# Performance work log

Hardware: AMD Instinct MI355X
Metric: run time of the kernel (lower is better)

## Reference

```python
import jax, jax.numpy as jnp
import numpy as np

B, N, C = 4, 2048, 512
H = 8  # num_heads
HD = C // H  # head_dim = 64


def setup_inputs() -> dict:
    key = jax.random.key(0)
    k_x, k_qkv, k_w, k_b = jax.random.split(key, 4)
    x = jax.random.normal(k_x, (B, N, C), dtype=jnp.float32)
    # torch nn.Linear weights are stored as (out_features, in_features)
    w_qkv = jax.random.normal(k_qkv, (3 * C, C), dtype=jnp.float32) * 0.02  # bias=False
    w_proj = jax.random.normal(k_w, (C, C), dtype=jnp.float32) * 0.02
    b_proj = jax.random.normal(k_b, (C,), dtype=jnp.float32) * 0.02
    return {"x": x, "w_qkv": w_qkv, "w_proj": w_proj, "b_proj": b_proj}


def reference(x, w_qkv, w_proj, b_proj):
    b, n, c = x.shape
    scale = HD ** -0.5
    # QKV projection (no bias): (B,N,C) @ (C,3C) -> (B,N,3C)
    qkv = jnp.einsum('bnc,dc->bnd', x, w_qkv)
    qkv = qkv.reshape(b, n, 3, H, HD).transpose(2, 0, 3, 1, 4)  # (3,B,H,N,HD)
    q, k, v = qkv[0], qkv[1], qkv[2]
    # scaled dot-product attention, full N x N scores
    attn = jnp.einsum('bhqd,bhkd->bhqk', q, k) * scale
    attn = jax.nn.softmax(attn, axis=-1)
    out = jnp.einsum('bhqk,bhkd->bhqd', attn, v)  # (B,H,N,HD)
    out = out.transpose(0, 2, 1, 3).reshape(b, n, c)  # (B,N,C)
    # output projection with bias
    return jnp.einsum('bnc,dc->bnd', out, w_proj) + b_proj
```

## Files before the change

kernel.cpp:

```cpp
#include <hip/hip_runtime.h>

typedef _Float16 f16;
typedef _Float16 f16x4 __attribute__((ext_vector_type(4)));
typedef _Float16 f16x8 __attribute__((ext_vector_type(8)));
typedef __fp16 fp16x2 __attribute__((ext_vector_type(2)));
typedef float f32x4 __attribute__((ext_vector_type(4)));

static __device__ __forceinline__ f32x4 mfma_k32(f16x8 a, f16x8 b, f32x4 c) {
  return __builtin_amdgcn_mfma_f32_16x16x32_f16(a, b, c, 0, 0, 0);
}
static __device__ __forceinline__ f32x4 mfma_k16(f16x4 a, f16x4 b, f32x4 c) {
  return __builtin_amdgcn_mfma_f32_16x16x16f16(a, b, c, 0, 0, 0);
}
static __device__ __forceinline__ void gll16(const f16* g, f16* l) {
  __builtin_amdgcn_global_load_lds(
      (const __attribute__((address_space(1))) void*)g,
      (__attribute__((address_space(3))) void*)l, 16, 0, 0);
}

#define BN 2048
#define CC 512
#define NHD 64
#define MROWS 8192
#define SLAB ((size_t)32 * BN * NHD)
#define CH 64
#define QSCALE 0.1803368801111204f

__global__ __launch_bounds__(256)
void cvt_f16(const float* __restrict__ X, const float* __restrict__ Wq,
             const float* __restrict__ Wp, f16* __restrict__ x16,
             f16* __restrict__ wq16, f16* __restrict__ wp16) {
  const int idx = blockIdx.x * 256 + threadIdx.x;
  const int stride = gridDim.x * 256;
  for (int i = idx; i < (MROWS * CC) / 4; i += stride) {
    float4 v = ((const float4*)X)[i];
    f16x4 h = {(f16)v.x, (f16)v.y, (f16)v.z, (f16)v.w};
    ((f16x4*)x16)[i] = h;
  }
  for (int i = idx; i < (3 * CC * CC) / 4; i += stride) {
    float4 v = ((const float4*)Wq)[i];
    f16x4 h = {(f16)v.x, (f16)v.y, (f16)v.z, (f16)v.w};
    ((f16x4*)wq16)[i] = h;
  }
  for (int i = idx; i < (CC * CC) / 4; i += stride) {
    float4 v = ((const float4*)Wp)[i];
    f16x4 h = {(f16)v.x, (f16)v.y, (f16)v.z, (f16)v.w};
    ((f16x4*)wp16)[i] = h;
  }
}

__global__ __launch_bounds__(256)
void qkv_gemm(const f16* __restrict__ X, const f16* __restrict__ W,
              f16* __restrict__ qkv) {
  __shared__ __align__(16) f16 As[128 * 32];
  __shared__ __align__(16) f16 Bs[128 * 32];
  const int t = threadIdx.x;
  const int lane = t & 63, wave = t >> 6;
  const int wr = wave >> 1, wc = wave & 1;
  const int mt = blockIdx.x / 12, nt = blockIdx.x % 12;
  const int m0 = mt * 128, n0 = nt * 128;
  const int grp = lane >> 4, lid = lane & 15;

  const int srow = 32 * wave + (lane >> 2);
  const int gslot = (lane & 3) ^ ((lane >> 2) & 3);
  const int ga0 = (m0 + srow) * CC + gslot * 8;
  const int gb0 = (n0 + srow) * CC + gslot * 8;
  f16* const ldsA = As + wave * 1024;
  f16* const ldsB = Bs + wave * 1024;

  const int abase = wr * 2048 + lid * 32 + (grp ^ (lid & 3)) * 8;
  const int bbase = wc * 2048 + lid * 32 + (grp ^ (lid & 3)) * 8;

  const f32x4 zf = {0.f, 0.f, 0.f, 0.f};
  f32x4 acc[4][4];
#pragma unroll
  for (int i = 0; i < 4; i++)
#pragma unroll
    for (int j = 0; j < 4; j++) acc[i][j] = zf;

  for (int k0 = 0; k0 < CC; k0 += 32) {
    gll16(X + ga0 + k0, ldsA);
    gll16(X + ga0 + 16 * CC + k0, ldsA + 512);
    gll16(W + gb0 + k0, ldsB);
    gll16(W + gb0 + 16 * CC + k0, ldsB + 512);
    __syncthreads();
    f16x8 af[4], bf[4];
#pragma unroll
    for (int mi = 0; mi < 4; mi++)
      af[mi] = *(const f16x8*)&As[abase + mi * 512];
#pragma unroll
    for (int ni = 0; ni < 4; ni++)
      bf[ni] = *(const f16x8*)&Bs[bbase + ni * 512];
#pragma unroll
    for (int mi = 0; mi < 4; mi++)
#pragma unroll
      for (int ni = 0; ni < 4; ni++)
        acc[mi][ni] = mfma_k32(af[mi], bf[ni], acc[mi][ni]);
    __syncthreads();
  }
#pragma unroll
  for (int ni = 0; ni < 4; ni++) {
    int d = n0 + wc * 64 + ni * 16 + lid;
    int s = d >> 9;
    int h = (d & 511) >> 6;
    int hd = d & 63;
    if (s == 2) {
#pragma unroll
      for (int mi = 0; mi < 4; mi++) {
        int row0 = m0 + wr * 64 + mi * 16 + grp * 4;
        int b = row0 >> 11, n = row0 & 2047;
        f16x4 pk = {(f16)acc[mi][ni][0], (f16)acc[mi][ni][1],
                    (f16)acc[mi][ni][2], (f16)acc[mi][ni][3]};
        *(f16x4*)&qkv[2 * SLAB + ((size_t)((b * 8 + h) * 64 + hd)) * BN + n] = pk;
      }
    } else {
      float scale = (s == 0) ? QSCALE : 1.0f;
#pragma unroll
      for (int mi = 0; mi < 4; mi++) {
#pragma unroll
        for (int i = 0; i < 4; i++) {
          int row = m0 + wr * 64 + mi * 16 + grp * 4 + i;
          int b = row >> 11, n = row & 2047;
          qkv[(size_t)s * SLAB + (((size_t)(b * 8 + h) * BN + n)) * NHD + hd] =
              (f16)(acc[mi][ni][i] * scale);
        }
      }
    }
  }
}

__global__ __launch_bounds__(256)
void attn(const f16* __restrict__ qkv, f16* __restrict__ O) {
  __shared__ __align__(16) char smem[32768];

  const int bh = blockIdx.x & 31;
  const int qb = blockIdx.x >> 5;
  const f16* Q = qkv + (size_t)bh * BN * NHD;
  const f16* K = qkv + SLAB + (size_t)bh * BN * NHD;
  const f16* VT = qkv + 2 * SLAB + (size_t)bh * (size_t)NHD * BN;
  const int t = threadIdx.x, lane = t & 63, wave = t >> 6;
  const int grp = lane >> 4, qv = lane & 15;
  const int qrow0 = qb * 128 + wave * 32 + qv;
  const int xr = (qv & 7) << 4;

  char* const kaddr0 = smem + qv * 128 + ((grp * 16) ^ xr);
  char* const kaddr1 = smem + qv * 128 + ((grp * 16 + 64) ^ xr);
  char* const va0 = smem + qv * 128 + ((0 * 32 + grp * 8) ^ xr);
  char* const va1 = smem + qv * 128 + ((1 * 32 + grp * 8) ^ xr);
  char* const va2 = smem + qv * 128 + ((2 * 32 + grp * 8) ^ xr);
  char* const va3 = smem + qv * 128 + ((3 * 32 + grp * 8) ^ xr);

  const int r0 = t >> 3, cb = t & 7, r1 = r0 + 32;
  const int lo_k0 = r0 * NHD + cb * 8;
  const int lo_k1 = r1 * NHD + cb * 8;
  const int lo_v0 = r0 * BN + cb * 8;
  const int lo_v1 = r1 * BN + cb * 8;
  char* const waddr0 = smem + ((r0 * 128 + cb * 16) ^ ((r0 & 7) << 4));
  char* const waddr1 = smem + ((r1 * 128 + cb * 16) ^ ((r1 & 7) << 4));

  f16x8 qfA0 = *(const f16x8*)(Q + (size_t)qrow0 * NHD + grp * 8);
  f16x8 qfA1 = *(const f16x8*)(Q + (size_t)qrow0 * NHD + 32 + grp * 8);
  f16x8 qfB0 = *(const f16x8*)(Q + (size_t)(qrow0 + 16) * NHD + grp * 8);
  f16x8 qfB1 = *(const f16x8*)(Q + (size_t)(qrow0 + 16) * NHD + 32 + grp * 8);

  const f32x4 zf = {0.f, 0.f, 0.f, 0.f};
  const f16x4 ones = {(f16)1.f, (f16)1.f, (f16)1.f, (f16)1.f};
  f32x4 accA[4], accB[4];
#pragma unroll
  for (int i = 0; i < 4; i++) { accA[i] = zf; accB[i] = zf; }
  f32x4 laccA = zf, laccB = zf;

  int koff = 0, voff = 0;
  {
    f16x8 sk0 = *(const f16x8*)(K + lo_k0);
    f16x8 sk1 = *(const f16x8*)(K + lo_k1);
    f16x8 sv0 = *(const f16x8*)(VT + lo_v0);
    f16x8 sv1 = *(const f16x8*)(VT + lo_v1);
    koff = CH * NHD; voff = CH;
    *(f16x8*)(waddr0) = sk0;
    *(f16x8*)(waddr1) = sk1;
    *(f16x8*)(waddr0 + 16384) = sv0;
    *(f16x8*)(waddr1 + 16384) = sv1;
  }
  __syncthreads();

#define ATTN_BODY(BUF, PF)                                                    \
  {                                                                           \
    f16x8 sk0, sk1, sv0, sv1;                                                 \
    if (PF) {                                                                 \
      sk0 = *(const f16x8*)(K + koff + lo_k0);                                \
      sk1 = *(const f16x8*)(K + koff + lo_k1);                                \
      sv0 = *(const f16x8*)(VT + voff + lo_v0);                               \
      sv1 = *(const f16x8*)(VT + voff + lo_v1);                               \
      koff += CH * NHD; voff += CH;                                           \
    }                                                                         \
    __builtin_amdgcn_s_setprio(1);                                            \
    _Pragma("unroll")                                                         \
    for (int kt = 0; kt < 4; kt++) {                                          \
      f16x8 k0v = *(const f16x8*)(kaddr0 + BUF * 8192 + kt * 2048);           \
      f16x8 k1v = *(const f16x8*)(kaddr1 + BUF * 8192 + kt * 2048);           \
      f32x4 stA = mfma_k32(k1v, qfA1, mfma_k32(k0v, qfA0, zf));               \
      f32x4 stB = mfma_k32(k1v, qfB1, mfma_k32(k0v, qfB0, zf));               \
      union { f16x4 v; fp16x2 h[2]; } uA, uB;                                 \
      uA.h[0] = __builtin_amdgcn_cvt_pkrtz(exp2f(stA[0]), exp2f(stA[1]));     \
      uA.h[1] = __builtin_amdgcn_cvt_pkrtz(exp2f(stA[2]), exp2f(stA[3]));     \
      uB.h[0] = __builtin_amdgcn_cvt_pkrtz(exp2f(stB[0]), exp2f(stB[1]));     \
      uB.h[1] = __builtin_amdgcn_cvt_pkrtz(exp2f(stB[2]), exp2f(stB[3]));     \
      f16x4 pbA = uA.v, pbB = uB.v;                                           \
      laccA = mfma_k16(ones, pbA, laccA);                                     \
      laccB = mfma_k16(ones, pbB, laccB);                                     \
      const char* vak = (kt == 0) ? va0 : (kt == 1) ? va1 : (kt == 2) ? va2 : va3; \
      _Pragma("unroll")                                                       \
      for (int dt = 0; dt < 4; dt++) {                                        \
        f16x4 vf = *(const f16x4*)(vak + 16384 + BUF * 8192 + dt * 2048);     \
        accA[dt] = mfma_k16(vf, pbA, accA[dt]);                               \
        accB[dt] = mfma_k16(vf, pbB, accB[dt]);                               \
      }                                                                       \
    }                                                                         \
    __builtin_amdgcn_s_setprio(0);                                            \
    if (PF) {                                                                 \
      *(f16x8*)(waddr0 + (BUF ^ 1) * 8192) = sk0;                             \
      *(f16x8*)(waddr1 + (BUF ^ 1) * 8192) = sk1;                             \
      *(f16x8*)(waddr0 + 16384 + (BUF ^ 1) * 8192) = sv0;                     \
      *(f16x8*)(waddr1 + 16384 + (BUF ^ 1) * 8192) = sv1;                     \
    }                                                                         \
    __syncthreads();                                                          \
  }

  for (int p = 0; p < 15; ++p) {
    ATTN_BODY(0, 1)
    ATTN_BODY(1, 1)
  }
  ATTN_BODY(0, 1)
  ATTN_BODY(1, 0)
#undef ATTN_BODY

  const int b = bh >> 3, h = bh & 7;
  {
    float inv = 1.0f / laccA[0];
#pragma unroll
    for (int dt = 0; dt < 4; dt++) {
      f16x4 o = {(f16)(accA[dt][0] * inv), (f16)(accA[dt][1] * inv),
                 (f16)(accA[dt][2] * inv), (f16)(accA[dt][3] * inv)};
      *(f16x4*)&O[((size_t)(b * BN + qrow0)) * CC + h * NHD + dt * 16 + grp * 4] = o;
    }
  }
  {
    float inv = 1.0f / laccB[0];
#pragma unroll
    for (int dt = 0; dt < 4; dt++) {
      f16x4 o = {(f16)(accB[dt][0] * inv), (f16)(accB[dt][1] * inv),
                 (f16)(accB[dt][2] * inv), (f16)(accB[dt][3] * inv)};
      *(f16x4*)&O[((size_t)(b * BN + qrow0 + 16)) * CC + h * NHD + dt * 16 + grp * 4] = o;
    }
  }
}

__global__ __launch_bounds__(256)
void proj_gemm(const f16* __restrict__ A, const f16* __restrict__ W,
               const float* __restrict__ bias, float* __restrict__ out) {
  __shared__ __align__(16) f16 As[128 * 32];
  __shared__ __align__(16) f16 Bs[128 * 32];
  const int t = threadIdx.x;
  const int lane = t & 63, wave = t >> 6;
  const int wr = wave >> 1, wc = wave & 1;
  const int mt = blockIdx.x >> 2, nt = blockIdx.x & 3;
  const int m0 = mt * 128, n0 = nt * 128;
  const int grp = lane >> 4, lid = lane & 15;

  const int srow = 32 * wave + (lane >> 2);
  const int gslot = (lane & 3) ^ ((lane >> 2) & 3);
  const int ga0 = (m0 + srow) * CC + gslot * 8;
  const int gb0 = (n0 + srow) * CC + gslot * 8;
  f16* const ldsA = As + wave * 1024;
  f16* const ldsB = Bs + wave * 1024;
  const int abase = wr * 2048 + lid * 32 + (grp ^ (lid & 3)) * 8;
  const int bbase = wc * 2048 + lid * 32 + (grp ^ (lid & 3)) * 8;

  const f32x4 zf = {0.f, 0.f, 0.f, 0.f};
  f32x4 acc[4][4];
#pragma unroll
  for (int i = 0; i < 4; i++)
#pragma unroll
    for (int j = 0; j < 4; j++) acc[i][j] = zf;

  for (int k0 = 0; k0 < CC; k0 += 32) {
    gll16(A + ga0 + k0, ldsA);
    gll16(A + ga0 + 16 * CC + k0, ldsA + 512);
    gll16(W + gb0 + k0, ldsB);
    gll16(W + gb0 + 16 * CC + k0, ldsB + 512);
    __syncthreads();
    f16x8 af[4], bf[4];
#pragma unroll
    for (int mi = 0; mi < 4; mi++)
      af[mi] = *(const f16x8*)&As[abase + mi * 512];
#pragma unroll
    for (int ni = 0; ni < 4; ni++)
      bf[ni] = *(const f16x8*)&Bs[bbase + ni * 512];
#pragma unroll
    for (int mi = 0; mi < 4; mi++)
#pragma unroll
      for (int ni = 0; ni < 4; ni++)
        acc[mi][ni] = mfma_k32(af[mi], bf[ni], acc[mi][ni]);
    __syncthreads();
  }
#pragma unroll
  for (int mi = 0; mi < 4; mi++) {
#pragma unroll
    for (int ni = 0; ni < 4; ni++) {
      int d = n0 + wc * 64 + ni * 16 + lid;
      float bv = bias[d];
#pragma unroll
      for (int i = 0; i < 4; i++) {
        int row = m0 + wr * 64 + mi * 16 + grp * 4 + i;
        out[(size_t)row * CC + d] = acc[mi][ni][i] + bv;
      }
    }
  }
}

extern "C" void kernel_launch(void* const* d_in, const int* in_sizes, int n_in,
                              void* d_out, int out_size, void* d_ws, size_t ws_size,
                              hipStream_t stream) {
  const float* x = (const float*)d_in[0];
  const float* w_qkv = (const float*)d_in[1];
  const float* w_proj = (const float*)d_in[2];
  const float* b_proj = (const float*)d_in[3];
  float* out = (float*)d_out;

  f16* qkv = (f16*)d_ws;
  f16* Obuf = qkv + 3 * SLAB;
  f16* x16 = Obuf;
  f16* wq16 = Obuf + (size_t)MROWS * CC;
  f16* wp16 = wq16 + (size_t)3 * CC * CC;

  cvt_f16<<<dim3(1024), dim3(256), 0, stream>>>(x, w_qkv, w_proj, x16, wq16, wp16);
  qkv_gemm<<<dim3(64 * 12), dim3(256), 0, stream>>>(x16, wq16, qkv);
  attn<<<dim3(16 * 32), dim3(256), 0, stream>>>(qkv, Obuf);
  proj_gemm<<<dim3(64 * 4), dim3(256), 0, stream>>>(Obuf, wp16, b_proj, out);
}
```

Baseline: 112.4 us.

## Split attention KV range in two and merge partials in a combine kernel

The attention kernel is split along the key dimension into two halves. This doubles the block count so more waves per CU are available to hide latency. Each half writes unnormalized f16 partial outputs and its row sums to workspace. A new combine kernel adds the two partials, normalizes them and scatters the result into the (B,N,C) layout. This adds an extra kernel launch and extra global traffic for the partials. Summing the partials without rescaling is only correct if both halves share the same softmax max offset.

```diff
diff --git a/kernel.cpp b/kernel.cpp
--- a/kernel.cpp
+++ b/kernel.cpp
@@ -24,6 +24,7 @@
 #define MROWS 8192
 #define SLAB ((size_t)32 * BN * NHD)
 #define CH 64
+#define KSPLIT 1024
 #define QSCALE 0.1803368801111204f
 
 __global__ __launch_bounds__(256)
@@ -130,14 +131,17 @@
 }
 
 __global__ __launch_bounds__(256)
-void attn(const f16* __restrict__ qkv, f16* __restrict__ O) {
+void attn_part(const f16* __restrict__ qkv, f16* __restrict__ part,
+               float* __restrict__ lpart) {
   __shared__ __align__(16) char smem[32768];
 
-  const int bh = blockIdx.x & 31;
-  const int qb = blockIdx.x >> 5;
+  const int bid = blockIdx.x;
+  const int split = bid >> 9;
+  const int bh = bid & 31;
+  const int qb = (bid >> 5) & 15;
   const f16* Q = qkv + (size_t)bh * BN * NHD;
-  const f16* K = qkv + SLAB + (size_t)bh * BN * NHD;
-  const f16* VT = qkv + 2 * SLAB + (size_t)bh * (size_t)NHD * BN;
+  const f16* K = qkv + SLAB + (size_t)bh * BN * NHD + (size_t)split * KSPLIT * NHD;
+  const f16* VT = qkv + 2 * SLAB + (size_t)bh * (size_t)NHD * BN + split * KSPLIT;
   const int t = threadIdx.x, lane = t & 63, wave = t >> 6;
   const int grp = lane >> 4, qv = lane & 15;
   const int qrow0 = qb * 128 + wave * 32 + qv;
@@ -227,7 +231,7 @@
     __syncthreads();                                                          \
   }
 
-  for (int p = 0; p < 15; ++p) {
+  for (int p = 0; p < 7; ++p) {
     ATTN_BODY(0, 1)
     ATTN_BODY(1, 1)
   }
@@ -235,25 +239,45 @@
   ATTN_BODY(1, 0)
 #undef ATTN_BODY
 
-  const int b = bh >> 3, h = bh & 7;
+  const size_t prow = (size_t)(split * 32 + bh) * BN;
   {
-    float inv = 1.0f / laccA[0];
+    size_t pbase = (prow + qrow0) * NHD;
 #pragma unroll
     for (int dt = 0; dt < 4; dt++) {
-      f16x4 o = {(f16)(accA[dt][0] * inv), (f16)(accA[dt][1] * inv),
-                 (f16)(accA[dt][2] * inv), (f16)(accA[dt][3] * inv)};
-      *(f16x4*)&O[((size_t)(b * BN + qrow0)) * CC + h * NHD + dt * 16 + grp * 4] = o;
+      f16x4 o = {(f16)accA[dt][0], (f16)accA[dt][1],
+                 (f16)accA[dt][2], (f16)accA[dt][3]};
+      *(f16x4*)&part[pbase + dt * 16 + grp * 4] = o;
     }
-  }
-  {
-    float inv = 1.0f / laccB[0];
+    pbase += (size_t)16 * NHD;
 #pragma unroll
     for (int dt = 0; dt < 4; dt++) {
-      f16x4 o = {(f16)(accB[dt][0] * inv), (f16)(accB[dt][1] * inv),
-                 (f16)(accB[dt][2] * inv), (f16)(accB[dt][3] * inv)};
-      *(f16x4*)&O[((size_t)(b * BN + qrow0 + 16)) * CC + h * NHD + dt * 16 + grp * 4] = o;
+      f16x4 o = {(f16)accB[dt][0], (f16)accB[dt][1],
+                 (f16)accB[dt][2], (f16)accB[dt][3]};
+      *(f16x4*)&part[pbase + dt * 16 + grp * 4] = o;
     }
   }
+  if (lane < 16) {
+    lpart[prow + qrow0] = laccA[0];
+    lpart[prow + qrow0 + 16] = laccB[0];
+  }
+}
+
+__global__ __launch_bounds__(256)
+void combine(const f16* __restrict__ part, const float* __restrict__ lpart,
+             f16* __restrict__ O) {
+  const int gid = blockIdx.x * 256 + threadIdx.x;
+  const int row = gid >> 3;
+  const int d0 = (gid & 7) * 8;
+  const float inv = 1.0f / (lpart[row] + lpart[(size_t)32 * BN + row]);
+  f16x8 a = *(const f16x8*)&part[(size_t)row * NHD + d0];
+  f16x8 b = *(const f16x8*)&part[((size_t)32 * BN + row) * NHD + d0];
+  f16x8 o;
+#pragma unroll
+  for (int i = 0; i < 8; i++)
+    o[i] = (f16)(((float)a[i] + (float)b[i]) * inv);
+  const int bh = row >> 11, n = row & 2047;
+  const int bb = bh >> 3, h = bh & 7;
+  *(f16x8*)&O[((size_t)(bb * BN + n)) * CC + h * NHD + d0] = o;
 }
 
 __global__ __launch_bounds__(256)
@@ -333,9 +357,12 @@
   f16* x16 = Obuf;
   f16* wq16 = Obuf + (size_t)MROWS * CC;
   f16* wp16 = wq16 + (size_t)3 * CC * CC;
+  f16* part = wp16 + (size_t)CC * CC;
+  float* lpart = (float*)(part + (size_t)2 * 32 * BN * NHD);
 
   cvt_f16<<<dim3(1024), dim3(256), 0, stream>>>(x, w_qkv, w_proj, x16, wq16, wp16);
   qkv_gemm<<<dim3(64 * 12), dim3(256), 0, stream>>>(x16, wq16, qkv);
-  attn<<<dim3(16 * 32), dim3(256), 0, stream>>>(qkv, Obuf);
+  attn_part<<<dim3(1024), dim3(256), 0, stream>>>(qkv, part, lpart);
+  combine<<<dim3(2048), dim3(256), 0, stream>>>(part, lpart, Obuf);
   proj_gemm<<<dim3(64 * 4), dim3(256), 0, stream>>>(Obuf, wp16, b_proj, out);
 }
```

After: 116.8 us. +3.9%, slower.
